# Optimization experiments

Measured on AMD Instinct MI355X. Metric: run time of the kernel, lower is better.

## Reference

```python
import jax, jax.numpy as jnp
import numpy as np

N_NODES = 20000
N_EDGES = 320000
VOCAB = 10000
D = 50          # F_in per tower (divide_input=False)
TOWERS = 5
F_OUT = 10      # out_channels // towers
N_LAYERS = 4
EPS_BN = 1e-5
EPS_STD = 1e-5


def setup_inputs() -> dict:
    key = jax.random.key(0)
    ks = jax.random.split(key, 24)
    rnd = lambda k, shape, s: (jax.random.normal(k, shape, jnp.float32) * s)
    inp = {
        "x": jax.random.randint(ks[0], (N_NODES,), 0, VOCAB, dtype=jnp.int32),
        "edge_index": jax.random.randint(ks[1], (2, N_EDGES), 0, N_NODES, dtype=jnp.int32),
        "edge_attr": jax.random.normal(ks[2], (N_EDGES, 4), jnp.float32),
        "batch": jnp.zeros((N_NODES,), jnp.int32),
        # parameters (stacked over the 4 conv layers)
        "emb": rnd(ks[3], (VOCAB, D), 1.0),
        "pre_W": rnd(ks[4], (N_LAYERS, TOWERS, D, 2 * D), 0.1),      # Linear(100,50) per tower
        "pre_b": rnd(ks[5], (N_LAYERS, TOWERS, D), 0.02),
        "post_W": rnd(ks[6], (N_LAYERS, TOWERS, F_OUT, 13 * D), 0.04),  # Linear(650,10) per tower
        "post_b": rnd(ks[7], (N_LAYERS, TOWERS, F_OUT), 0.02),
        "lin_W": rnd(ks[8], (N_LAYERS, D, D), 0.14),                 # Linear(50,50)
        "lin_b": rnd(ks[9], (N_LAYERS, D), 0.02),
        "bn_gamma": jnp.ones((N_LAYERS, D), jnp.float32),
        "bn_beta": jnp.zeros((N_LAYERS, D), jnp.float32),
        "mlp_W1": rnd(ks[10], (25, D), 0.14),
        "mlp_b1": rnd(ks[11], (25,), 0.02),
        "mlp_W2": rnd(ks[12], (1, 25), 0.2),
        "mlp_b2": rnd(ks[13], (1,), 0.02),
    }
    return inp


def _pna_conv(xh, src, dst, deg, avg_log, Wpre, bpre, Wpost, bpost, Wlin, blin):
    # xh: [N, D]. Pre-NN Linear(2D, D) per tower, applied to cat([x_i, x_j]).
    # Split the weight so we never materialize the [E, T, 2D] concat tensor.
    ai = jnp.einsum('nf,tgf->ntg', xh, Wpre[:, :, :D])   # x_i (target) part, [N,T,D]
    aj = jnp.einsum('nf,tgf->ntg', xh, Wpre[:, :, D:])   # x_j (source) part, [N,T,D]
    msg = ai[dst] + aj[src] + bpre[None]                 # [E,T,D]

    cnt = jnp.maximum(deg, 1.0)[:, None, None]           # clamped degree, [N,1,1]
    mean = jax.ops.segment_sum(msg, dst, N_NODES) / cnt
    mean_sq = jax.ops.segment_sum(msg * msg, dst, N_NODES) / cnt
    std = jnp.sqrt(jax.nn.relu(mean_sq - mean * mean) + EPS_STD)
    mn = jax.ops.segment_min(msg, dst, N_NODES)
    mx = jax.ops.segment_max(msg, dst, N_NODES)
    empty = (deg == 0)[:, None, None]                    # torch_scatter fills empties with 0
    mn = jnp.where(empty, 0.0, mn)
    mx = jnp.where(empty, 0.0, mx)

    agg = jnp.concatenate([mean, mn, mx, std], axis=-1)  # [N,T,4D] (aggregator order)
    sc = jnp.log(cnt + 1.0) / avg_log                    # amplification scaler
    out = jnp.concatenate([agg, agg * sc, agg / sc], axis=-1)   # identity/amp/atten -> [N,T,12D]

    xt = jnp.broadcast_to(xh[:, None, :], (xh.shape[0], TOWERS, D))
    h = jnp.concatenate([xt, out], axis=-1)              # [N,T,13D]
    y = jnp.einsum('ntf,tgf->ntg', h, Wpost) + bpost[None]  # post-NN per tower, [N,T,F_OUT]
    y = y.reshape(-1, TOWERS * F_OUT)                    # [N,50]
    return y @ Wlin.T + blin


def reference(x, edge_index, edge_attr, batch, emb, pre_W, pre_b, post_W, post_b,
              lin_W, lin_b, bn_gamma, bn_beta, mlp_W1, mlp_b1, mlp_W2, mlp_b2):
    src, dst = edge_index[0], edge_index[1]              # flow source_to_target
    deg = jax.ops.segment_sum(jnp.ones((src.shape[0],), jnp.float32), dst, N_NODES)
    avg_log = jnp.mean(jnp.log(deg + 1.0))               # PNA avg_deg['log'] from this graph

    h = emb[x]                                           # [N,D]
    for l in range(N_LAYERS):
        h = _pna_conv(h, src, dst, deg, avg_log, pre_W[l], pre_b[l],
                      post_W[l], post_b[l], lin_W[l], lin_b[l])
        mu = h.mean(axis=0)
        var = h.var(axis=0)                              # biased, as BatchNorm1d (train)
        h = jax.nn.relu(bn_gamma[l] * (h - mu) / jnp.sqrt(var + EPS_BN) + bn_beta[l])

    z = jax.nn.relu(h @ mlp_W1.T + mlp_b1)
    return jax.nn.sigmoid(z @ mlp_W2.T + mlp_b2)         # [N,1]
```

## Files before the change

### kernel.cpp

```cpp
#include <hip/hip_runtime.h>
#include <hip/hip_fp16.h>
#include <math.h>

#define NN 20000
#define NNP 20224
#define NGRP3 316
#define NE 320000
#define D 50
#define TOWERS 5
#define TD 250
#define ASTR 256
#define FOUT 10
#define EPS 1e-5f

__global__ void k_deg(const int* __restrict__ dst, int* __restrict__ deg) {
    int e = blockIdx.x * 256 + threadIdx.x;
    if (e < NE) atomicAdd(&deg[dst[e]], 1);
}

__global__ __launch_bounds__(256) void k_hist(const int* __restrict__ deg,
                                              int* __restrict__ hist) {
    __shared__ int lh[256];
    int tid = threadIdx.x;
    lh[tid] = 0;
    __syncthreads();
    int n = blockIdx.x * 256 + tid;
    if (n < NN) atomicAdd(&lh[min(deg[n], 255)], 1);
    __syncthreads();
    if (lh[tid] > 0) atomicAdd(&hist[tid], lh[tid]);
}

__global__ void k_binscan(const int* __restrict__ hist, int* __restrict__ binbase,
                          int* __restrict__ ebase, float* __restrict__ avglog_out) {
    __shared__ int b[256];
    __shared__ int eb[256];
    __shared__ float lg[256];
    int tid = threadIdx.x;
    int h = hist[tid];
    b[tid] = h;
    eb[tid] = h * tid;
    lg[tid] = (float)h * logf((float)tid + 1.0f);
    __syncthreads();
    for (int off = 1; off < 256; off <<= 1) {
        int t1 = (tid >= off) ? b[tid - off] : 0;
        int t2 = (tid >= off) ? eb[tid - off] : 0;
        float t3 = (tid >= off) ? lg[tid - off] : 0.f;
        __syncthreads();
        b[tid] += t1; eb[tid] += t2; lg[tid] += t3;
        __syncthreads();
    }
    binbase[tid] = b[tid] - h;
    ebase[tid] = eb[tid] - h * tid;
    if (tid == 255) avglog_out[0] = lg[255];
}

__global__ __launch_bounds__(256) void k_scatter(
    const int* __restrict__ deg, const int* __restrict__ binbase,
    int* __restrict__ cursorb, int* __restrict__ perm,
    int* __restrict__ invp, int* __restrict__ deg_r) {
    __shared__ int lh[256];
    __shared__ int lbase[256];
    int tid = threadIdx.x;
    lh[tid] = 0;
    __syncthreads();
    int n = blockIdx.x * 256 + tid;
    int d = 0, slot = 0;
    bool ok = n < NN;
    if (ok) {
        d = min(deg[n], 255);
        slot = atomicAdd(&lh[d], 1);
    }
    __syncthreads();
    if (lh[tid] > 0) lbase[tid] = atomicAdd(&cursorb[tid], lh[tid]);
    __syncthreads();
    if (ok) {
        int r = binbase[d] + lbase[d] + slot;
        perm[r] = n;
        invp[n] = r;
        deg_r[r] = deg[n];
    }
}

__global__ void k_offs(const int* __restrict__ deg_r, const int* __restrict__ binbase,
                       const int* __restrict__ ebase, int* __restrict__ offs) {
    int r = blockIdx.x * 256 + threadIdx.x;
    if (r < NN) {
        int d = deg_r[r];
        int dc = min(d, 255);
        offs[r] = ebase[dc] + (r - binbase[dc]) * d;
    }
    if (r == 0) offs[NN] = NE;
}

__global__ void k_csr(const int* __restrict__ src, const int* __restrict__ dst,
                      const int* __restrict__ offs, const int* __restrict__ invp,
                      int* __restrict__ cursor, int* __restrict__ csr_src) {
    int e = blockIdx.x * 256 + threadIdx.x;
    if (e < NE) {
        int rd = invp[dst[e]];
        int slot = atomicAdd(&cursor[rd], 1);
        csr_src[offs[rd] + slot] = invp[src[e]];
    }
}

__global__ void k_emb(const int* __restrict__ x, const float* __restrict__ emb,
                      const int* __restrict__ perm, float* __restrict__ hT) {
    int idx = blockIdx.x * 256 + threadIdx.x;
    if (idx < D * NNP) {
        int c = idx / NNP, r = idx % NNP;
        hT[idx] = (r < NN) ? emb[x[perm[r]] * D + c] : 0.f;
    }
}

__global__ void k_wt(const float* __restrict__ postW, float* __restrict__ wT,
                     float* __restrict__ wxT) {
    int idx = blockIdx.x * 256 + threadIdx.x;
    const int WTN = 4 * TOWERS * 200 * 32;
    if (idx < WTN) {
        int l = idx / (TOWERS * 200 * 32);
        int r = idx % (TOWERS * 200 * 32);
        int t = r / (200 * 32); r %= 200 * 32;
        int j = r / 32, c = r % 32;
        float v = 0.f;
        if (c < 30) {
            int p = c / 10, g = c % 10;
            v = postW[l * 32500 + (t * FOUT + g) * 650 + 50 + p * 200 + j];
        }
        wT[idx] = v;
    } else if (idx < WTN + 4 * TOWERS * 50 * 16) {
        int k = idx - WTN;
        int l = k / (TOWERS * 50 * 16);
        int r = k % (TOWERS * 50 * 16);
        int t = r / (50 * 16); r %= 50 * 16;
        int j = r / 16, c = r % 16;
        float v = 0.f;
        if (c < 10) v = postW[l * 32500 + (t * FOUT + c) * 650 + j];
        wxT[k] = v;
    }
}

#define PRE_NT 16
__global__ __launch_bounds__(512) void k_pre(const float* __restrict__ hT,
                                             const float* __restrict__ preW,
                                             __half* __restrict__ aih,
                                             __half* __restrict__ ajh) {
    __shared__ float xl[PRE_NT * 52];
    int n0 = blockIdx.x * PRE_NT;
    int tid = threadIdx.x;
    for (int k = tid; k < PRE_NT * 52; k += 512) {
        int nl = k & 15, f = k >> 4;
        xl[nl * 52 + f] = (f < 50) ? hT[(size_t)f * NNP + n0 + nl] : 0.f;
    }
    __syncthreads();
    int isj = tid >> 8;
    int oo = tid & 255;
    __half* dstp = isj ? ajh : aih;
    if (oo < 250) {
        const float* w0 = preW + oo * 100 + isj * 50;
        float w[52];
#pragma unroll
        for (int f = 0; f < 50; ++f) w[f] = w0[f];
        w[50] = 0.f; w[51] = 0.f;
        for (int nl = 0; nl < PRE_NT; ++nl) {
            const float4* xv = (const float4*)&xl[nl * 52];
            float a0 = 0.f, a1 = 0.f, a2 = 0.f, a3 = 0.f;
#pragma unroll
            for (int j = 0; j < 12; j += 4) {
                float4 xa = xv[j], xb = xv[j + 1], xc = xv[j + 2], xd = xv[j + 3];
                a0 = fmaf(xa.x, w[4*j],   a0); a0 = fmaf(xa.y, w[4*j+1], a0);
                a0 = fmaf(xa.z, w[4*j+2], a0); a0 = fmaf(xa.w, w[4*j+3], a0);
                a1 = fmaf(xb.x, w[4*j+4], a1); a1 = fmaf(xb.y, w[4*j+5], a1);
                a1 = fmaf(xb.z, w[4*j+6], a1); a1 = fmaf(xb.w, w[4*j+7], a1);
                a2 = fmaf(xc.x, w[4*j+8], a2); a2 = fmaf(xc.y, w[4*j+9], a2);
                a2 = fmaf(xc.z, w[4*j+10], a2); a2 = fmaf(xc.w, w[4*j+11], a2);
                a3 = fmaf(xd.x, w[4*j+12], a3); a3 = fmaf(xd.y, w[4*j+13], a3);
                a3 = fmaf(xd.z, w[4*j+14], a3); a3 = fmaf(xd.w, w[4*j+15], a3);
            }
            float4 xe = xv[12];
            a0 = fmaf(xe.x, w[48], a0); a1 = fmaf(xe.y, w[49], a1);
            a2 = fmaf(xe.z, w[50], a2); a3 = fmaf(xe.w, w[51], a3);
            float a = (a0 + a1) + (a2 + a3);
            dstp[(size_t)(n0 + nl) * ASTR + oo] = __float2half(a);
        }
    } else {
        for (int nl = 0; nl < PRE_NT; ++nl)
            dstp[(size_t)(n0 + nl) * ASTR + oo] = __float2half(0.f);
    }
}

__global__ __launch_bounds__(512) void k_agg(
    const __half* __restrict__ aj, const int* __restrict__ offs,
    const int* __restrict__ csr_src, const __half* __restrict__ ai,
    const float* __restrict__ preB, __half* __restrict__ aggT) {
    int chunk = blockIdx.x & 3;
    int nb = (gridDim.x >> 2) - 1 - (blockIdx.x >> 2);
    int tid = threadIdx.x;
    int wave = tid >> 6, lane = tid & 63;
    int g = lane >> 3, q = lane & 7;
    int r = nb * 64 + wave * 8 + g;
    int coloff = chunk * 8 + q;
    bool ok = r < NN;
    int e0 = 0, dg = 0;
    if (ok) { e0 = offs[r]; dg = offs[r + 1] - e0; }
    int mdeg = dg;
#pragma unroll
    for (int o = 8; o < 64; o <<= 1) mdeg = min(mdeg, __shfl_xor(mdeg, o));

    const float4* ajv = (const float4*)aj;
    float s1[8], s2[8], mn[8], mx[8];
#pragma unroll
    for (int k = 0; k < 8; ++k) {
        s1[k] = 0.f; s2[k] = 0.f; mn[k] = INFINITY; mx[k] = -INFINITY;
    }

    int nblk = mdeg >> 2;
    int spref[4];
    if (nblk > 0) {
#pragma unroll
        for (int k = 0; k < 4; ++k) spref[k] = csr_src[e0 + k];
    }
    for (int b = 0; b < nblk; ++b) {
        int scur[4];
#pragma unroll
        for (int k = 0; k < 4; ++k) scur[k] = spref[k];
        int nxt = (b + 1 < nblk) ? (b + 1) * 4 : 0;
#pragma unroll
        for (int k = 0; k < 4; ++k) spref[k] = csr_src[e0 + nxt + k];
        float4 raw[4];
#pragma unroll
        for (int k = 0; k < 4; ++k)
            raw[k] = ajv[((unsigned)scur[k] << 5) + coloff];
#pragma unroll
        for (int k = 0; k < 4; ++k) {
            const __half2* hp = (const __half2*)&raw[k];
#pragma unroll
            for (int j = 0; j < 4; ++j) {
                float2 f = __half22float2(hp[j]);
                s1[2*j]   += f.x; s2[2*j]   = fmaf(f.x, f.x, s2[2*j]);
                mn[2*j]   = fminf(mn[2*j], f.x); mx[2*j]   = fmaxf(mx[2*j], f.x);
                s1[2*j+1] += f.y; s2[2*j+1] = fmaf(f.y, f.y, s2[2*j+1]);
                mn[2*j+1] = fminf(mn[2*j+1], f.y); mx[2*j+1] = fmaxf(mx[2*j+1], f.y);
            }
        }
    }
    int it = nblk << 2;
    for (; it < mdeg; ++it) {
        float4 raw = ajv[((unsigned)csr_src[e0 + it] << 5) + coloff];
        const __half2* hp = (const __half2*)&raw;
#pragma unroll
        for (int j = 0; j < 4; ++j) {
            float2 f = __half22float2(hp[j]);
            s1[2*j]   += f.x; s2[2*j]   = fmaf(f.x, f.x, s2[2*j]);
            mn[2*j]   = fminf(mn[2*j], f.x); mx[2*j]   = fmaxf(mx[2*j], f.x);
            s1[2*j+1] += f.y; s2[2*j+1] = fmaf(f.y, f.y, s2[2*j+1]);
            mn[2*j+1] = fminf(mn[2*j+1], f.y); mx[2*j+1] = fmaxf(mx[2*j+1], f.y);
        }
    }
    while (__any(it < dg)) {
        bool valid = it < dg;
        float4 raw = ajv[((unsigned)csr_src[valid ? e0 + it : e0] << 5) + coloff];
        const __half2* hp = (const __half2*)&raw;
#pragma unroll
        for (int j = 0; j < 4; ++j) {
            float2 f = __half22float2(hp[j]);
            float vx = valid ? f.x : 0.f, vy = valid ? f.y : 0.f;
            s1[2*j]   += vx; s2[2*j]   = fmaf(vx, vx, s2[2*j]);
            mn[2*j]   = fminf(mn[2*j], valid ? f.x : INFINITY);
            mx[2*j]   = fmaxf(mx[2*j], valid ? f.x : -INFINITY);
            s1[2*j+1] += vy; s2[2*j+1] = fmaf(vy, vy, s2[2*j+1]);
            mn[2*j+1] = fminf(mn[2*j+1], valid ? f.y : INFINITY);
            mx[2*j+1] = fmaxf(mx[2*j+1], valid ? f.y : -INFINITY);
        }
        ++it;
    }

    if (ok) {
        float inv = 1.0f / (float)max(dg, 1);
        float4 aihr = ((const float4*)ai)[(size_t)r * 32 + coloff];
        const __half2* ap = (const __half2*)&aihr;
        int f0 = coloff * 8;
#pragma unroll
        for (int j = 0; j < 4; ++j) {
            float2 av = __half22float2(ap[j]);
            float aval[2] = {av.x, av.y};
#pragma unroll
            for (int h = 0; h < 2; ++h) {
                int k = 2 * j + h;
                int f = f0 + k;
                if (f < TD) {
                    float m1 = s1[k] * inv;
                    float sd = sqrtf(fmaxf(s2[k] * inv - m1 * m1, 0.f) + EPS);
                    float mm, mnv, mxv;
                    if (dg > 0) {
                        float base = aval[h] + preB[f];
                        mm = m1 + base; mnv = mn[k] + base; mxv = mx[k] + base;
                    } else {
                        mm = 0.f; mnv = 0.f; mxv = 0.f; sd = sqrtf(EPS);
                    }
                    int t = f / 50, gg = f - t * 50;
                    __half* col = aggT + (size_t)(t * 200 + gg) * NNP + r;
                    col[0]                 = __float2half(mm);
                    col[(size_t)50 * NNP]  = __float2half(mnv);
                    col[(size_t)100 * NNP] = __float2half(mxv);
                    col[(size_t)150 * NNP] = __float2half(sd);
                }
            }
        }
    }
}

__global__ __launch_bounds__(256) void k_post(
    const float* __restrict__ hT, const __half* __restrict__ aggT,
    const int* __restrict__ offs,
    const float* __restrict__ wT,
    const float* __restrict__ wxT,
    const float* __restrict__ postB,
    const float* __restrict__ avg_accum, float* __restrict__ yT) {
    __shared__ float dp[3][64][33];
    int t = blockIdx.x / NGRP3;
    int grp = blockIdx.x - t * NGRP3;
    int tid = threadIdx.x;
    int qd = tid >> 6, ln = tid & 63;
    int qdu = __builtin_amdgcn_readfirstlane(qd);
    int n = grp * 64 + ln;

    float acc[30];
#pragma unroll
    for (int i = 0; i < 30; ++i) acc[i] = 0.f;
    const __half* aggcol = aggT + (size_t)(t * 200) * NNP + n;
    const float4* wv = (const float4*)(wT + t * 200 * 32);
    int j0 = qdu * 50;
    int j1 = j0 + 50;
#pragma unroll 4
    for (int j = j0; j < j1; ++j) {
        float a = __half2float(aggcol[(size_t)j * NNP]);
        float4 w0 = wv[j * 8 + 0], w1 = wv[j * 8 + 1], w2 = wv[j * 8 + 2],
               w3 = wv[j * 8 + 3], w4 = wv[j * 8 + 4], w5 = wv[j * 8 + 5],
               w6 = wv[j * 8 + 6], w7 = wv[j * 8 + 7];
        acc[0] = fmaf(a, w0.x, acc[0]);   acc[1] = fmaf(a, w0.y, acc[1]);
        acc[2] = fmaf(a, w0.z, acc[2]);   acc[3] = fmaf(a, w0.w, acc[3]);
        acc[4] = fmaf(a, w1.x, acc[4]);   acc[5] = fmaf(a, w1.y, acc[5]);
        acc[6] = fmaf(a, w1.z, acc[6]);   acc[7] = fmaf(a, w1.w, acc[7]);
        acc[8] = fmaf(a, w2.x, acc[8]);   acc[9] = fmaf(a, w2.y, acc[9]);
        acc[10] = fmaf(a, w2.z, acc[10]); acc[11] = fmaf(a, w2.w, acc[11]);
        acc[12] = fmaf(a, w3.x, acc[12]); acc[13] = fmaf(a, w3.y, acc[13]);
        acc[14] = fmaf(a, w3.z, acc[14]); acc[15] = fmaf(a, w3.w, acc[15]);
        acc[16] = fmaf(a, w4.x, acc[16]); acc[17] = fmaf(a, w4.y, acc[17]);
        acc[18] = fmaf(a, w4.z, acc[18]); acc[19] = fmaf(a, w4.w, acc[19]);
        acc[20] = fmaf(a, w5.x, acc[20]); acc[21] = fmaf(a, w5.y, acc[21]);
        acc[22] = fmaf(a, w5.z, acc[22]); acc[23] = fmaf(a, w5.w, acc[23]);
        acc[24] = fmaf(a, w6.x, acc[24]); acc[25] = fmaf(a, w6.y, acc[25]);
        acc[26] = fmaf(a, w6.z, acc[26]); acc[27] = fmaf(a, w6.w, acc[27]);
        acc[28] = fmaf(a, w7.x, acc[28]); acc[29] = fmaf(a, w7.y, acc[29]);
    }
    float xacc[10];
#pragma unroll
    for (int i = 0; i < 10; ++i) xacc[i] = 0.f;
    if (qdu == 0) {
        const float4* wxv = (const float4*)(wxT + t * 50 * 16);
#pragma unroll 2
        for (int j = 0; j < 50; ++j) {
            float a = hT[(size_t)j * NNP + n];
            float4 x0 = wxv[j * 4 + 0], x1 = wxv[j * 4 + 1], x2 = wxv[j * 4 + 2];
            xacc[0] = fmaf(a, x0.x, xacc[0]); xacc[1] = fmaf(a, x0.y, xacc[1]);
            xacc[2] = fmaf(a, x0.z, xacc[2]); xacc[3] = fmaf(a, x0.w, xacc[3]);
            xacc[4] = fmaf(a, x1.x, xacc[4]); xacc[5] = fmaf(a, x1.y, xacc[5]);
            xacc[6] = fmaf(a, x1.z, xacc[6]); xacc[7] = fmaf(a, x1.w, xacc[7]);
            xacc[8] = fmaf(a, x2.x, xacc[8]); xacc[9] = fmaf(a, x2.y, xacc[9]);
        }
    } else {
#pragma unroll
        for (int g = 0; g < 30; ++g) dp[qdu - 1][ln][g] = acc[g];
    }
    __syncthreads();
    if (qd == 0 && n < NN) {
        int dgn = offs[n + 1] - offs[n];
        float cnt = (float)max(dgn, 1);
        float sc = logf(cnt + 1.0f) / (avg_accum[0] * (1.0f / NN));
        float isc = 1.0f / sc;
#pragma unroll
        for (int g = 0; g < 10; ++g) {
            float a0 = acc[g]      + dp[0][ln][g]      + dp[1][ln][g]      + dp[2][ln][g];
            float a1 = acc[10 + g] + dp[0][ln][10 + g] + dp[1][ln][10 + g] + dp[2][ln][10 + g];
            float a2 = acc[20 + g] + dp[0][ln][20 + g] + dp[1][ln][20 + g] + dp[2][ln][20 + g];
            yT[(size_t)(t * FOUT + g) * NNP + n] =
                postB[t * FOUT + g] + xacc[g] + a0 + sc * a1 + isc * a2;
        }
    }
}

__global__ __launch_bounds__(256) void k_lin(
    const float* __restrict__ yT, const float* __restrict__ linW,
    const float* __restrict__ linB, float* __restrict__ hrawT) {
    __shared__ float wl[2500];
    __shared__ float bl[50];
    int tid = threadIdx.x;
    int n = blockIdx.x * 256 + tid;
    for (int i = tid; i < 2500; i += 256) wl[i] = linW[i];
    if (tid < 50) bl[tid] = linB[tid];
    __syncthreads();
    float y[50];
#pragma unroll
    for (int q = 0; q < 50; ++q) y[q] = yT[(size_t)q * NNP + n];
    for (int c = 0; c < 50; ++c) {
        float a = bl[c];
        const float* w = wl + c * 50;
#pragma unroll
        for (int q = 0; q < 50; ++q) a = fmaf(w[q], y[q], a);
        hrawT[(size_t)c * NNP + n] = a;
    }
}

__global__ __launch_bounds__(256) void k_bnstats(const float* __restrict__ hrawT,
                                                 float* __restrict__ bn) {
    int c = blockIdx.x;
    int tid = threadIdx.x;
    const float* row = hrawT + (size_t)c * NNP;
    float s = 0.f, sq = 0.f;
    for (int n = tid; n < NN; n += 256) {
        float v = row[n];
        s += v; sq = fmaf(v, v, sq);
    }
    for (int o = 32; o > 0; o >>= 1) {
        s += __shfl_down(s, o);
        sq += __shfl_down(sq, o);
    }
    __shared__ float ws[4], wq[4];
    int lane = tid & 63, w = tid >> 6;
    if (lane == 0) { ws[w] = s; wq[w] = sq; }
    __syncthreads();
    if (tid == 0) {
        bn[c] = ws[0] + ws[1] + ws[2] + ws[3];
        bn[50 + c] = wq[0] + wq[1] + wq[2] + wq[3];
    }
}

__global__ void k_bnapply(const float* __restrict__ hrawT, const float* __restrict__ bn,
                          const float* __restrict__ gamma, const float* __restrict__ beta,
                          float* __restrict__ hT) {
    int idx = blockIdx.x * 256 + threadIdx.x;
    if (idx < D * NNP) {
        int c = idx / NNP, n = idx % NNP;
        float mean = bn[c] * (1.0f / NN);
        float var = bn[50 + c] * (1.0f / NN) - mean * mean;
        float v = gamma[c] * (hrawT[idx] - mean) * rsqrtf(var + EPS) + beta[c];
        hT[idx] = (n < NN) ? fmaxf(v, 0.f) : 0.f;
    }
}

__global__ void k_mlp(const float* __restrict__ hT, const int* __restrict__ perm,
                      const float* __restrict__ W1, const float* __restrict__ b1,
                      const float* __restrict__ W2, const float* __restrict__ b2,
                      float* __restrict__ out) {
    int n = blockIdx.x * 256 + threadIdx.x;
    if (n >= NN) return;
    float hv[50];
#pragma unroll
    for (int f = 0; f < 50; ++f) hv[f] = hT[(size_t)f * NNP + n];
    float s = b2[0];
    for (int o = 0; o < 25; ++o) {
        float a = b1[o];
        const float* w = W1 + o * 50;
#pragma unroll
        for (int f = 0; f < 50; ++f) a += w[f] * hv[f];
        s += W2[o] * fmaxf(a, 0.f);
    }
    out[perm[n]] = 1.0f / (1.0f + expf(-s));
}

extern "C" void kernel_launch(void* const* d_in, const int* in_sizes, int n_in,
                              void* d_out, int out_size, void* d_ws, size_t ws_size,
                              hipStream_t stream) {
    const int* x = (const int*)d_in[0];
    const int* ei = (const int*)d_in[1];
    const int* src = ei;
    const int* dst = ei + NE;
    const float* emb   = (const float*)d_in[4];
    const float* preW  = (const float*)d_in[5];
    const float* preB  = (const float*)d_in[6];
    const float* postW = (const float*)d_in[7];
    const float* postB = (const float*)d_in[8];
    const float* linW  = (const float*)d_in[9];
    const float* linB  = (const float*)d_in[10];
    const float* gamma = (const float*)d_in[11];
    const float* beta  = (const float*)d_in[12];
    const float* W1 = (const float*)d_in[13];
    const float* b1 = (const float*)d_in[14];
    const float* W2 = (const float*)d_in[15];
    const float* b2 = (const float*)d_in[16];
    float* outp = (float*)d_out;

    char* wsp = (char*)d_ws;
    size_t off = 0;
    auto alloc = [&](size_t bytes) {
        void* p = wsp + off;
        off = (off + bytes + 1023) & ~(size_t)1023;
        return p;
    };
    int* deg     = (int*)alloc(NN * 4);
    int* cursor  = (int*)alloc(NN * 4);
    int* offs    = (int*)alloc((NN + 1) * 4);
    int* csr     = (int*)alloc(NE * 4);
    int* perm    = (int*)alloc(NN * 4);
    int* invp    = (int*)alloc(NN * 4);
    int* deg_r   = (int*)alloc(NN * 4);
    int* hist    = (int*)alloc(256 * 4);
    int* binbase = (int*)alloc(256 * 4);
    int* ebase   = (int*)alloc(256 * 4);
    int* cursorb = (int*)alloc(256 * 4);
    float* bn    = (float*)alloc(512);
    float* hT    = (float*)alloc((size_t)D * NNP * 4);
    float* hrawT = (float*)alloc((size_t)D * NNP * 4);
    float* yT    = (float*)alloc((size_t)D * NNP * 4);
    __half* aih  = (__half*)alloc((size_t)NN * ASTR * 2);
    __half* ajh  = (__half*)alloc((size_t)NN * ASTR * 2);
    float* wT    = (float*)alloc((size_t)4 * TOWERS * 200 * 32 * 4);
    float* wxT   = (float*)alloc((size_t)4 * TOWERS * 50 * 16 * 4);
    __half* aggT = (__half*)alloc((size_t)1000 * NNP * 2);
    (void)ws_size; (void)in_sizes; (void)n_in; (void)out_size;

    hipMemsetAsync(deg, 0, NN * 4, stream);
    hipMemsetAsync(cursor, 0, NN * 4, stream);
    hipMemsetAsync(hist, 0, 256 * 4, stream);
    hipMemsetAsync(cursorb, 0, 256 * 4, stream);
    hipMemsetAsync(bn, 0, 512, stream);

    k_deg<<<(NE + 255) / 256, 256, 0, stream>>>(dst, deg);
    k_hist<<<(NN + 255) / 256, 256, 0, stream>>>(deg, hist);
    k_binscan<<<1, 256, 0, stream>>>(hist, binbase, ebase, bn + 100);
    k_scatter<<<(NN + 255) / 256, 256, 0, stream>>>(deg, binbase, cursorb, perm, invp, deg_r);
    k_offs<<<(NN + 255) / 256, 256, 0, stream>>>(deg_r, binbase, ebase, offs);
    k_csr<<<(NE + 255) / 256, 256, 0, stream>>>(src, dst, offs, invp, cursor, csr);
    k_emb<<<(D * NNP + 255) / 256, 256, 0, stream>>>(x, emb, perm, hT);
    k_wt<<<(4 * TOWERS * 200 * 32 + 4 * TOWERS * 50 * 16 + 255) / 256, 256, 0, stream>>>(postW, wT, wxT);

    int aggblocks = 313 * 4;
    for (int l = 0; l < 4; ++l) {
        k_pre<<<NN / PRE_NT, 512, 0, stream>>>(hT, preW + l * TD * 100, aih, ajh);
        k_agg<<<aggblocks, 512, 0, stream>>>(ajh, offs, csr, aih, preB + l * TD, aggT);
        k_post<<<NGRP3 * TOWERS, 256, 0, stream>>>(hT, aggT, offs,
                                                   wT + l * TOWERS * 200 * 32,
                                                   wxT + l * TOWERS * 50 * 16,
                                                   postB + l * 50, bn + 100, yT);
        k_lin<<<NNP / 256, 256, 0, stream>>>(yT, linW + l * 2500, linB + l * 50, hrawT);
        k_bnstats<<<50, 256, 0, stream>>>(hrawT, bn);
        k_bnapply<<<(D * NNP + 255) / 256, 256, 0, stream>>>(hrawT, bn, gamma + l * 50,
                                                             beta + l * 50, hT);
    }
    k_mlp<<<(NN + 255) / 256, 256, 0, stream>>>(hT, perm, W1, b1, W2, b2, outp);
}
```

Measured before the change: 653.4 us.

## Fuse BN statistics into linear kernel, merge offs into scatter, rebalance post loads

Merges the CSR offset computation into the scatter kernel, which removes one launch and the deg_r buffer. In the post-tower kernel, the aggregate loads are batched ten at a time so they overlap better, and the skip-projection work moves from wave 0 to wave 1 and is passed through shared memory. The linear kernel now stages 64 nodes of y in LDS, splits output channels across waves, and computes per-block sum and sum-of-squares partials, so a small reduce kernel replaces the full re-read of hrawT for batch-norm stats. The cost is an extra partial buffer and a two-stage reduction. Weight reads in k_lin now come from global or scalar memory instead of LDS.

```diff
diff --git a/kernel.cpp b/kernel.cpp
--- a/kernel.cpp
+++ b/kernel.cpp
@@ -56,8 +56,8 @@
 
 __global__ __launch_bounds__(256) void k_scatter(
     const int* __restrict__ deg, const int* __restrict__ binbase,
-    int* __restrict__ cursorb, int* __restrict__ perm,
-    int* __restrict__ invp, int* __restrict__ deg_r) {
+    const int* __restrict__ ebase, int* __restrict__ cursorb,
+    int* __restrict__ perm, int* __restrict__ invp, int* __restrict__ offs) {
     __shared__ int lh[256];
     __shared__ int lbase[256];
     int tid = threadIdx.x;
@@ -77,19 +77,9 @@
         int r = binbase[d] + lbase[d] + slot;
         perm[r] = n;
         invp[n] = r;
-        deg_r[r] = deg[n];
-    }
-}
-
-__global__ void k_offs(const int* __restrict__ deg_r, const int* __restrict__ binbase,
-                       const int* __restrict__ ebase, int* __restrict__ offs) {
-    int r = blockIdx.x * 256 + threadIdx.x;
-    if (r < NN) {
-        int d = deg_r[r];
-        int dc = min(d, 255);
-        offs[r] = ebase[dc] + (r - binbase[dc]) * d;
-    }
-    if (r == 0) offs[NN] = NE;
+        offs[r] = ebase[d] + (r - binbase[d]) * d;
+    }
+    if (n == 0) offs[NN] = NE;
 }
 
 __global__ void k_csr(const int* __restrict__ src, const int* __restrict__ dst,
@@ -317,6 +307,7 @@
     const float* __restrict__ postB,
     const float* __restrict__ avg_accum, float* __restrict__ yT) {
     __shared__ float dp[3][64][33];
+    __shared__ float xs[64][11];
     int t = blockIdx.x / NGRP3;
     int grp = blockIdx.x - t * NGRP3;
     int tid = threadIdx.x;
@@ -330,45 +321,61 @@
     const __half* aggcol = aggT + (size_t)(t * 200) * NNP + n;
     const float4* wv = (const float4*)(wT + t * 200 * 32);
     int j0 = qdu * 50;
-    int j1 = j0 + 50;
-#pragma unroll 4
-    for (int j = j0; j < j1; ++j) {
-        float a = __half2float(aggcol[(size_t)j * NNP]);
-        float4 w0 = wv[j * 8 + 0], w1 = wv[j * 8 + 1], w2 = wv[j * 8 + 2],
-               w3 = wv[j * 8 + 3], w4 = wv[j * 8 + 4], w5 = wv[j * 8 + 5],
-               w6 = wv[j * 8 + 6], w7 = wv[j * 8 + 7];
-        acc[0] = fmaf(a, w0.x, acc[0]);   acc[1] = fmaf(a, w0.y, acc[1]);
-        acc[2] = fmaf(a, w0.z, acc[2]);   acc[3] = fmaf(a, w0.w, acc[3]);
-        acc[4] = fmaf(a, w1.x, acc[4]);   acc[5] = fmaf(a, w1.y, acc[5]);
-        acc[6] = fmaf(a, w1.z, acc[6]);   acc[7] = fmaf(a, w1.w, acc[7]);
-        acc[8] = fmaf(a, w2.x, acc[8]);   acc[9] = fmaf(a, w2.y, acc[9]);
-        acc[10] = fmaf(a, w2.z, acc[10]); acc[11] = fmaf(a, w2.w, acc[11]);
-        acc[12] = fmaf(a, w3.x, acc[12]); acc[13] = fmaf(a, w3.y, acc[13]);
-        acc[14] = fmaf(a, w3.z, acc[14]); acc[15] = fmaf(a, w3.w, acc[15]);
-        acc[16] = fmaf(a, w4.x, acc[16]); acc[17] = fmaf(a, w4.y, acc[17]);
-        acc[18] = fmaf(a, w4.z, acc[18]); acc[19] = fmaf(a, w4.w, acc[19]);
-        acc[20] = fmaf(a, w5.x, acc[20]); acc[21] = fmaf(a, w5.y, acc[21]);
-        acc[22] = fmaf(a, w5.z, acc[22]); acc[23] = fmaf(a, w5.w, acc[23]);
-        acc[24] = fmaf(a, w6.x, acc[24]); acc[25] = fmaf(a, w6.y, acc[25]);
-        acc[26] = fmaf(a, w6.z, acc[26]); acc[27] = fmaf(a, w6.w, acc[27]);
-        acc[28] = fmaf(a, w7.x, acc[28]); acc[29] = fmaf(a, w7.y, acc[29]);
-    }
-    float xacc[10];
-#pragma unroll
-    for (int i = 0; i < 10; ++i) xacc[i] = 0.f;
-    if (qdu == 0) {
+    for (int b = 0; b < 5; ++b) {
+        float av[10];
+#pragma unroll
+        for (int k = 0; k < 10; ++k)
+            av[k] = __half2float(aggcol[(size_t)(j0 + b * 10 + k) * NNP]);
+#pragma unroll
+        for (int k = 0; k < 10; ++k) {
+            int j = j0 + b * 10 + k;
+            float a = av[k];
+            float4 w0 = wv[j * 8 + 0], w1 = wv[j * 8 + 1], w2 = wv[j * 8 + 2],
+                   w3 = wv[j * 8 + 3], w4 = wv[j * 8 + 4], w5 = wv[j * 8 + 5],
+                   w6 = wv[j * 8 + 6], w7 = wv[j * 8 + 7];
+            acc[0] = fmaf(a, w0.x, acc[0]);   acc[1] = fmaf(a, w0.y, acc[1]);
+            acc[2] = fmaf(a, w0.z, acc[2]);   acc[3] = fmaf(a, w0.w, acc[3]);
+            acc[4] = fmaf(a, w1.x, acc[4]);   acc[5] = fmaf(a, w1.y, acc[5]);
+            acc[6] = fmaf(a, w1.z, acc[6]);   acc[7] = fmaf(a, w1.w, acc[7]);
+            acc[8] = fmaf(a, w2.x, acc[8]);   acc[9] = fmaf(a, w2.y, acc[9]);
+            acc[10] = fmaf(a, w2.z, acc[10]); acc[11] = fmaf(a, w2.w, acc[11]);
+            acc[12] = fmaf(a, w3.x, acc[12]); acc[13] = fmaf(a, w3.y, acc[13]);
+            acc[14] = fmaf(a, w3.z, acc[14]); acc[15] = fmaf(a, w3.w, acc[15]);
+            acc[16] = fmaf(a, w4.x, acc[16]); acc[17] = fmaf(a, w4.y, acc[17]);
+            acc[18] = fmaf(a, w4.z, acc[18]); acc[19] = fmaf(a, w4.w, acc[19]);
+            acc[20] = fmaf(a, w5.x, acc[20]); acc[21] = fmaf(a, w5.y, acc[21]);
+            acc[22] = fmaf(a, w5.z, acc[22]); acc[23] = fmaf(a, w5.w, acc[23]);
+            acc[24] = fmaf(a, w6.x, acc[24]); acc[25] = fmaf(a, w6.y, acc[25]);
+            acc[26] = fmaf(a, w6.z, acc[26]); acc[27] = fmaf(a, w6.w, acc[27]);
+            acc[28] = fmaf(a, w7.x, acc[28]); acc[29] = fmaf(a, w7.y, acc[29]);
+        }
+    }
+    if (qdu == 1) {
+        float xacc[10];
+#pragma unroll
+        for (int i = 0; i < 10; ++i) xacc[i] = 0.f;
         const float4* wxv = (const float4*)(wxT + t * 50 * 16);
-#pragma unroll 2
-        for (int j = 0; j < 50; ++j) {
-            float a = hT[(size_t)j * NNP + n];
-            float4 x0 = wxv[j * 4 + 0], x1 = wxv[j * 4 + 1], x2 = wxv[j * 4 + 2];
-            xacc[0] = fmaf(a, x0.x, xacc[0]); xacc[1] = fmaf(a, x0.y, xacc[1]);
-            xacc[2] = fmaf(a, x0.z, xacc[2]); xacc[3] = fmaf(a, x0.w, xacc[3]);
-            xacc[4] = fmaf(a, x1.x, xacc[4]); xacc[5] = fmaf(a, x1.y, xacc[5]);
-            xacc[6] = fmaf(a, x1.z, xacc[6]); xacc[7] = fmaf(a, x1.w, xacc[7]);
-            xacc[8] = fmaf(a, x2.x, xacc[8]); xacc[9] = fmaf(a, x2.y, xacc[9]);
-        }
-    } else {
+        for (int b = 0; b < 5; ++b) {
+            float av[10];
+#pragma unroll
+            for (int k = 0; k < 10; ++k)
+                av[k] = hT[(size_t)(b * 10 + k) * NNP + n];
+#pragma unroll
+            for (int k = 0; k < 10; ++k) {
+                int j = b * 10 + k;
+                float a = av[k];
+                float4 x0 = wxv[j * 4 + 0], x1 = wxv[j * 4 + 1], x2 = wxv[j * 4 + 2];
+                xacc[0] = fmaf(a, x0.x, xacc[0]); xacc[1] = fmaf(a, x0.y, xacc[1]);
+                xacc[2] = fmaf(a, x0.z, xacc[2]); xacc[3] = fmaf(a, x0.w, xacc[3]);
+                xacc[4] = fmaf(a, x1.x, xacc[4]); xacc[5] = fmaf(a, x1.y, xacc[5]);
+                xacc[6] = fmaf(a, x1.z, xacc[6]); xacc[7] = fmaf(a, x1.w, xacc[7]);
+                xacc[8] = fmaf(a, x2.x, xacc[8]); xacc[9] = fmaf(a, x2.y, xacc[9]);
+            }
+        }
+#pragma unroll
+        for (int g = 0; g < 10; ++g) xs[ln][g] = xacc[g];
+    }
+    if (qdu != 0) {
 #pragma unroll
         for (int g = 0; g < 30; ++g) dp[qdu - 1][ln][g] = acc[g];
     }
@@ -384,55 +391,60 @@
             float a1 = acc[10 + g] + dp[0][ln][10 + g] + dp[1][ln][10 + g] + dp[2][ln][10 + g];
             float a2 = acc[20 + g] + dp[0][ln][20 + g] + dp[1][ln][20 + g] + dp[2][ln][20 + g];
             yT[(size_t)(t * FOUT + g) * NNP + n] =
-                postB[t * FOUT + g] + xacc[g] + a0 + sc * a1 + isc * a2;
+                postB[t * FOUT + g] + xs[ln][g] + a0 + sc * a1 + isc * a2;
         }
     }
 }
 
 __global__ __launch_bounds__(256) void k_lin(
     const float* __restrict__ yT, const float* __restrict__ linW,
-    const float* __restrict__ linB, float* __restrict__ hrawT) {
-    __shared__ float wl[2500];
-    __shared__ float bl[50];
-    int tid = threadIdx.x;
-    int n = blockIdx.x * 256 + tid;
-    for (int i = tid; i < 2500; i += 256) wl[i] = linW[i];
-    if (tid < 50) bl[tid] = linB[tid];
-    __syncthreads();
-    float y[50];
-#pragma unroll
-    for (int q = 0; q < 50; ++q) y[q] = yT[(size_t)q * NNP + n];
-    for (int c = 0; c < 50; ++c) {
-        float a = bl[c];
-        const float* w = wl + c * 50;
-#pragma unroll
-        for (int q = 0; q < 50; ++q) a = fmaf(w[q], y[q], a);
+    const float* __restrict__ linB, float* __restrict__ hrawT,
+    float* __restrict__ part) {
+    __shared__ float yl[64][51];
+    __shared__ float bs[100];
+    int tid = threadIdx.x;
+    int n0 = blockIdx.x * 64;
+    for (int idx = tid; idx < 64 * 50; idx += 256) {
+        int q = idx >> 6, nl = idx & 63;
+        yl[nl][q] = yT[(size_t)q * NNP + n0 + nl];
+    }
+    __syncthreads();
+    int w = tid >> 6, nl = tid & 63;
+    int wu = __builtin_amdgcn_readfirstlane(w);
+    int n = n0 + nl;
+    bool ok = n < NN;
+    int c0 = wu * 13, c1 = min(50, c0 + 13);
+    for (int c = c0; c < c1; ++c) {
+        const float* wr = linW + c * 50;
+        float a = linB[c];
+#pragma unroll
+        for (int q = 0; q < 50; ++q) a = fmaf(wr[q], yl[nl][q], a);
         hrawT[(size_t)c * NNP + n] = a;
-    }
-}
-
-__global__ __launch_bounds__(256) void k_bnstats(const float* __restrict__ hrawT,
-                                                 float* __restrict__ bn) {
+        float s = ok ? a : 0.f;
+        float sq = s * s;
+#pragma unroll
+        for (int o = 32; o > 0; o >>= 1) {
+            s += __shfl_down(s, o);
+            sq += __shfl_down(sq, o);
+        }
+        if (nl == 0) { bs[c] = s; bs[50 + c] = sq; }
+    }
+    __syncthreads();
+    if (tid < 100) part[blockIdx.x * 100 + tid] = bs[tid];
+}
+
+__global__ __launch_bounds__(256) void k_bnred(const float* __restrict__ part,
+                                               float* __restrict__ bn) {
     int c = blockIdx.x;
     int tid = threadIdx.x;
-    const float* row = hrawT + (size_t)c * NNP;
-    float s = 0.f, sq = 0.f;
-    for (int n = tid; n < NN; n += 256) {
-        float v = row[n];
-        s += v; sq = fmaf(v, v, sq);
-    }
-    for (int o = 32; o > 0; o >>= 1) {
-        s += __shfl_down(s, o);
-        sq += __shfl_down(sq, o);
-    }
-    __shared__ float ws[4], wq[4];
+    float s = 0.f;
+    for (int b = tid; b < NGRP3; b += 256) s += part[b * 100 + c];
+    for (int o = 32; o > 0; o >>= 1) s += __shfl_down(s, o);
+    __shared__ float ws[4];
     int lane = tid & 63, w = tid >> 6;
-    if (lane == 0) { ws[w] = s; wq[w] = sq; }
-    __syncthreads();
-    if (tid == 0) {
-        bn[c] = ws[0] + ws[1] + ws[2] + ws[3];
-        bn[50 + c] = wq[0] + wq[1] + wq[2] + wq[3];
-    }
+    if (lane == 0) ws[w] = s;
+    __syncthreads();
+    if (tid == 0) bn[c] = ws[0] + ws[1] + ws[2] + ws[3];
 }
 
 __global__ void k_bnapply(const float* __restrict__ hrawT, const float* __restrict__ bn,
@@ -503,12 +515,12 @@
     int* csr     = (int*)alloc(NE * 4);
     int* perm    = (int*)alloc(NN * 4);
     int* invp    = (int*)alloc(NN * 4);
-    int* deg_r   = (int*)alloc(NN * 4);
     int* hist    = (int*)alloc(256 * 4);
     int* binbase = (int*)alloc(256 * 4);
     int* ebase   = (int*)alloc(256 * 4);
     int* cursorb = (int*)alloc(256 * 4);
     float* bn    = (float*)alloc(512);
+    float* part  = (float*)alloc((size_t)NGRP3 * 100 * 4);
     float* hT    = (float*)alloc((size_t)D * NNP * 4);
     float* hrawT = (float*)alloc((size_t)D * NNP * 4);
     float* yT    = (float*)alloc((size_t)D * NNP * 4);
@@ -528,8 +540,8 @@
     k_deg<<<(NE + 255) / 256, 256, 0, stream>>>(dst, deg);
     k_hist<<<(NN + 255) / 256, 256, 0, stream>>>(deg, hist);
     k_binscan<<<1, 256, 0, stream>>>(hist, binbase, ebase, bn + 100);
-    k_scatter<<<(NN + 255) / 256, 256, 0, stream>>>(deg, binbase, cursorb, perm, invp, deg_r);
-    k_offs<<<(NN + 255) / 256, 256, 0, stream>>>(deg_r, binbase, ebase, offs);
+    k_scatter<<<(NN + 255) / 256, 256, 0, stream>>>(deg, binbase, ebase, cursorb,
+                                                    perm, invp, offs);
     k_csr<<<(NE + 255) / 256, 256, 0, stream>>>(src, dst, offs, invp, cursor, csr);
     k_emb<<<(D * NNP + 255) / 256, 256, 0, stream>>>(x, emb, perm, hT);
     k_wt<<<(4 * TOWERS * 200 * 32 + 4 * TOWERS * 50 * 16 + 255) / 256, 256, 0, stream>>>(postW, wT, wxT);
@@ -542,8 +554,8 @@
                                                    wT + l * TOWERS * 200 * 32,
                                                    wxT + l * TOWERS * 50 * 16,
                                                    postB + l * 50, bn + 100, yT);
-        k_lin<<<NNP / 256, 256, 0, stream>>>(yT, linW + l * 2500, linB + l * 50, hrawT);
-        k_bnstats<<<50, 256, 0, stream>>>(hrawT, bn);
+        k_lin<<<NGRP3, 256, 0, stream>>>(yT, linW + l * 2500, linB + l * 50, hrawT, part);
+        k_bnred<<<100, 256, 0, stream>>>(part, bn);
         k_bnapply<<<(D * NNP + 255) / 256, 256, 0, stream>>>(hrawT, bn, gamma + l * 50,
                                                              beta + l * 50, hT);
     }
```

Result: faster. 551.1 us (-15.6%).
